# Kernel tuning notes

Measured on AMD Instinct MI355X. Metric: run time of the kernel, lower is better.

Reference implementation:

```python
import jax, jax.numpy as jnp
import numpy as np

B = 256          # batch
MID = 16384      # mid_siz
OUT = 16384      # out_siz
C = 16           # channel_siz
NLVL = 8         # nlvl (== klvl here since floor(log2(OUT/2))=13 >= 8)
MIDF = MID >> NLVL   # mid_filter_siz = 64
OUTF = OUT >> NLVL   # out_filter_siz = 64
NB = 1 << NLVL       # 256 leaf branches
STD = 0.5


def setup_inputs() -> dict:
    key = jax.random.key(0)
    ks = jax.random.split(key, 6)
    in_data = jax.random.normal(ks[0], (B, MID, 2), jnp.float32)
    # learned parameters (buildRand: normal(0, 0.5) filters, zero biases)
    mid_dense = jax.random.normal(ks[1], (1, MID, 2), jnp.float32) * STD
    in_filter = jax.random.normal(ks[2], (MIDF, 1, C), jnp.float32) * STD   # conv1d [width,in,out]
    in_bias = jnp.zeros((C,), jnp.float32)
    # level lvl (1..NLVL) uses filters[lvl-1, :2**lvl]; padded to NB branches
    filters = jax.random.normal(ks[3], (NLVL, NB, 2, C, C), jnp.float32) * STD
    biases = jnp.zeros((NLVL, NB, C), jnp.float32)
    fea_dense = jax.random.normal(ks[4], (NB, C, OUTF), jnp.float32) * STD
    return dict(in_data=in_data, mid_dense=mid_dense, in_filter=in_filter,
                in_bias=in_bias, filters=filters, biases=biases, fea_dense=fea_dense)


def reference(in_data, mid_dense, in_filter, in_bias, filters, biases, fea_dense):
    # elementwise modulation then split real/imag channels: (B, 2, MID)
    x = jnp.moveaxis(in_data * mid_dense, -1, 1)
    # level-0 conv1d: kernel MIDF, stride MIDF//2 -> overlapping half-windows.
    # Split signal into half-width chunks h; window t = [h[t], h[t+1]].
    half = MIDF // 2
    h = x.reshape(B, 2, MID // half, half)                 # (B,2,512,32)
    W1 = in_filter[:half, 0, :]                            # (32,C)
    W2 = in_filter[half:, 0, :]
    s = jnp.einsum('bisw,wc->bisc', h[:, :, :-1], W1) \
        + jnp.einsum('bisw,wc->bisc', h[:, :, 1:], W2)
    s = jax.nn.relu(s + in_bias)                           # (B,2,2^(n+1)-1,C)
    state = s[:, :, None]                                  # (B,2,nb=1,L,C)
    # butterfly tree: each level doubles branches; conv kernel=2, stride=2, VALID
    for lvl in range(1, NLVL + 1):
        nb = 1 << lvl
        p = jnp.repeat(state, 2, axis=2)                   # child itk <- parent itk//2
        L = p.shape[3]                                     # odd: 2^(n+1-lvl+1)-1
        xw = p[:, :, :, :L - 1, :].reshape(B, 2, nb, (L - 1) // 2, 2, C)
        W = filters[lvl - 1, :nb]                          # (nb,2,C,C)
        bb = biases[lvl - 1, :nb]                          # (nb,C)
        state = jax.nn.relu(
            jnp.einsum('bintkc,nkcd->bintd', xw, W) + bb[None, None, :, None, :])
    feat = state[:, :, :, 0, :]                            # (B,2,NB,C): L==1 at last level
    outp = jnp.einsum('binc,ncf->binf', feat, fea_dense)   # per-branch dense projection
    R = outp[:, 0].reshape(B, OUT // 2, 2)
    I = outp[:, 1].reshape(B, OUT // 2, 2)
    out_data = ((R[:, :, 0] - I[:, :, 1]) / MID).reshape(B, OUT // 2, 1)
    return out_data, R[:, :, 1]
```

## Files before the change

### kernel.cpp

```cpp
#include <hip/hip_runtime.h>


#define OUT_HALF 2097152

typedef __attribute__((ext_vector_type(4))) float f32x4;
typedef __attribute__((ext_vector_type(8))) short s16x8;

__device__ __forceinline__ uint fsw(uint a) {
    return a ^ ((((a >> 6) ^ (a >> 8)) & 3u) << 4);
}
__device__ __forceinline__ ushort bfr(float f) {
    uint u = __float_as_uint(f);
    return (ushort)((u + 0x7FFFu + ((u >> 16) & 1u)) >> 16);
}
__device__ __forceinline__ uint pk(float a, float b) {
    return (uint)bfr(a) | ((uint)bfr(b) << 16);
}

__device__ __forceinline__ void tree_level(
    char* smb, const int lane, const int wave,
    uint AOff, uint NOff, int lgR, int lgNP, int nTiles,
    uint WOff, int wnb, uint LBOff, int bnb)
{
    const int m  = lane & 15;
    const int kg = lane >> 4;
    const int lgTPP = lgR - 4;
    for (int at = wave; at < nTiles; at += 4) {
        const int p  = at >> lgTPP;
        const int tc = at & ((1 << lgTPP) - 1);
        const int np = p & ((1 << lgNP) - 1);
        const int ii = p >> lgNP;
        s16x8 af = *(const s16x8*)(smb + AOff + (p << (lgR + 6)) +
                                   fsw((uint)((tc * 16 + m) * 64 + kg * 16)));
#pragma unroll
        for (int sib = 0; sib < 2; sib++) {
            const int nl = 2 * np + sib;
            s16x8 bf = *(const s16x8*)(smb + WOff +
                         fsw((uint)((wnb + nl) * 1024 + m * 64 + kg * 16)));
            float bv = *(const float*)(smb + LBOff + ((bnb + nl) * 16 + m) * 4);
            f32x4 acc = {bv, bv, bv, bv};
            acc = __builtin_amdgcn_mfma_f32_16x16x32_bf16(af, bf, acc, 0, 0, 0);
            const int p2 = (ii << (lgNP + 1)) + nl;
            const uint wb = NOff + (p2 << (lgR + 5));
            const int r2 = tc * 8 + kg * 2;
            *(uint*)(smb + wb + fsw((uint)(r2 * 64 + m * 4))) =
                pk(fmaxf(acc.x, 0.f), fmaxf(acc.y, 0.f));
            *(uint*)(smb + wb + fsw((uint)((r2 + 1) * 64 + m * 4))) =
                pk(fmaxf(acc.z, 0.f), fmaxf(acc.w, 0.f));
        }
    }
}

__global__ __launch_bounds__(256, 3)
void ibf_A(const float* __restrict__ in_data, const float* __restrict__ mid_dense,
           const float* __restrict__ in_filter, const float* __restrict__ in_bias,
           const float* __restrict__ filters, const float* __restrict__ biases,
           uint* __restrict__ S3)
{
    __shared__ __align__(16) char smb[42048];
    const int tid = threadIdx.x, lane = tid & 63, wave = tid >> 6;
    const int b = blockIdx.x, th = blockIdx.y;

    {
        const float4* inb = (const float4*)in_data + (size_t)b * 8192 + th * 2048;
        const float4* mdb = (const float4*)mid_dense + th * 2048;
        for (int mp = tid; mp < 2064; mp += 256) {
            float4 iv = inb[mp], mv = mdb[mp];
            *(uint*)(smb + 0    + fsw((uint)(mp * 4))) = pk(iv.x * mv.x, iv.z * mv.z);
            *(uint*)(smb + 8256 + fsw((uint)(mp * 4))) = pk(iv.y * mv.y, iv.w * mv.w);
        }
    }
    for (int t = tid; t < 3584; t += 256) {
        int nidx = t >> 8, r = t & 255, d = r & 15, c = r >> 4;
        int lvl = (nidx < 2) ? 1 : ((nidx < 6) ? 2 : 3);
        int n = nidx - ((1 << lvl) - 2);
        const float* src = filters + (size_t)(lvl - 1) * 131072 + n * 512 + c * 16 + d;
        *(uint*)(smb + 24704 + fsw((uint)(nidx * 1024 + d * 64 + c * 4))) = pk(src[0], src[256]);
    }
    for (int t = tid; t < 512; t += 256) {
        int c = t >> 5, w2 = t & 31;
        *(uint*)(smb + 39040 + fsw((uint)(c * 128 + w2 * 4))) =
            pk(in_filter[(2 * w2) * 16 + c], in_filter[(2 * w2 + 1) * 16 + c]);
    }
    if (tid < 240) {
        float v;
        if (tid < 224) {
            int nidx = tid >> 4;
            int lvl = (nidx < 2) ? 1 : ((nidx < 6) ? 2 : 3);
            int n = nidx - ((1 << lvl) - 2);
            v = biases[(size_t)(lvl - 1) * 4096 + n * 16 + (tid & 15)];
        } else v = in_bias[tid - 224];
        *(float*)(smb + 41088 + tid * 4) = v;
    }
    __syncthreads();

    {
        const int m = lane & 15, kg = lane >> 4;
        s16x8 b0 = *(const s16x8*)(smb + 39040 + fsw((uint)(m * 128 + kg * 16)));
        s16x8 b1 = *(const s16x8*)(smb + 39040 + fsw((uint)(m * 128 + 64 + kg * 16)));
        float bv = *(const float*)(smb + 41088 + (224 + m) * 4);
        for (int at = wave; at < 16; at += 4) {
            int i = at >> 3, tc = at & 7;
            uint xb = i ? 8256u : 0u;
            s16x8 a0 = *(const s16x8*)(smb + xb + fsw((uint)((tc * 16 + m) * 64 + kg * 16)));
            s16x8 a1 = *(const s16x8*)(smb + xb + fsw((uint)((tc * 16 + m) * 64 + 64 + kg * 16)));
            f32x4 acc = {bv, bv, bv, bv};
            acc = __builtin_amdgcn_mfma_f32_16x16x32_bf16(a0, b0, acc, 0, 0, 0);
            acc = __builtin_amdgcn_mfma_f32_16x16x32_bf16(a1, b1, acc, 0, 0, 0);
            uint wb = 16512u + (uint)i * 4096u;
            int r2 = tc * 8 + kg * 2;
            *(uint*)(smb + wb + fsw((uint)(r2 * 64 + m * 4))) =
                pk(fmaxf(acc.x, 0.f), fmaxf(acc.y, 0.f));
            *(uint*)(smb + wb + fsw((uint)((r2 + 1) * 64 + m * 4))) =
                pk(fmaxf(acc.z, 0.f), fmaxf(acc.w, 0.f));
        }
    }
    __syncthreads();
    tree_level(smb, lane, wave, 16512, 0,    6, 0, 8, 24704, 0, 41088, 0);
    __syncthreads();
    tree_level(smb, lane, wave, 0,     8256, 5, 1, 8, 24704, 2, 41088, 2);
    __syncthreads();
    {
        const int m = lane & 15, kg = lane >> 4;
        for (int at = wave; at < 8; at += 4) {
            int np = at & 3, i = at >> 2;
            s16x8 af = *(const s16x8*)(smb + 8256 + (at << 10) + fsw((uint)(m * 64 + kg * 16)));
#pragma unroll
            for (int sib = 0; sib < 2; sib++) {
                int n3 = 2 * np + sib;
                s16x8 bf = *(const s16x8*)(smb + 24704 +
                             fsw((uint)((6 + n3) * 1024 + m * 64 + kg * 16)));
                float bv = *(const float*)(smb + 41088 + ((6 + n3) * 16 + m) * 4);
                f32x4 acc = {bv, bv, bv, bv};
                acc = __builtin_amdgcn_mfma_f32_16x16x32_bf16(af, bf, acc, 0, 0, 0);
                int bi = 2 * b + i;
                int t4 = th * 8 + kg * 2;
                uint idx = ((uint)(n3 * 512 + bi) * 16 + t4) * 16 + m;
                S3[idx]      = pk(fmaxf(acc.x, 0.f), fmaxf(acc.y, 0.f));
                S3[idx + 16] = pk(fmaxf(acc.z, 0.f), fmaxf(acc.w, 0.f));
            }
        }
    }
}

__global__ __launch_bounds__(256, 2)
void ibf_B(const float* __restrict__ filters, const float* __restrict__ biases,
           const float* __restrict__ fea_dense, const uint* __restrict__ S3,
           float* __restrict__ out)
{
    __shared__ __align__(16) char smb[69504];
    const int tid = threadIdx.x, lane = tid & 63, wave = tid >> 6;
    const int n3 = blockIdx.x, chunk = blockIdx.y;

    for (int o = tid * 16; o < 16384; o += 4096)
        *(float4*)(smb + 16384 + o) = make_float4(0.f, 0.f, 0.f, 0.f);
    {
        const char* src = (const char*)S3 + ((size_t)n3 * 512 + chunk * 8) * 1024;
        for (int ci = tid; ci < 512; ci += 256)
            *(float4*)(smb + fsw((uint)(ci * 16))) = *(const float4*)(src + ci * 16);
    }
    for (int t = tid; t < 992; t += 256) {
        int nidx = t >> 4, q = nidx + 2;
        int l3 = 31 - __clz(q);
        int nl = q - (1 << l3);
        int gn = (n3 << l3) + nl;
        *(float*)(smb + 65536 + t * 4) = biases[(size_t)(l3 + 2) * 4096 + gn * 16 + (t & 15)];
    }
    auto stage_w = [&](int l3) {
        int NL = 1 << l3;
        const float* fb = filters + (size_t)(l3 + 2) * 131072;
        for (int t = tid; t < NL * 256; t += 256) {
            int nl = t >> 8, r = t & 255, d = r & 15, c = r >> 4;
            const float* src = fb + (size_t)((n3 << l3) + nl) * 512 + c * 16 + d;
            *(uint*)(smb + 32768 + fsw((uint)(nl * 1024 + d * 64 + c * 4))) = pk(src[0], src[256]);
        }
    };
    stage_w(1);
    __syncthreads();
    tree_level(smb, lane, wave, 0,    8192, 7, 0, 8, 32768, 0, 65536, 0);
    __syncthreads();
    stage_w(2);
    __syncthreads();
    tree_level(smb, lane, wave, 8192, 0,    6, 1, 8, 32768, 0, 65536, 2);
    __syncthreads();
    stage_w(3);
    __syncthreads();
    tree_level(smb, lane, wave, 0,    8192, 5, 2, 8, 32768, 0, 65536, 6);
    __syncthreads();
    stage_w(4);
    __syncthreads();
    tree_level(smb, lane, wave, 8192, 0,    4, 3, 8, 32768, 0, 65536, 14);
    __syncthreads();
    stage_w(5);
    __syncthreads();
    {
        const int m = lane & 15, kg = lane >> 4;
        for (int at = wave; at < 16; at += 4) {
            s16x8 af = *(const s16x8*)(smb + at * 512 + fsw((uint)(m * 64 + kg * 16)));
#pragma unroll
            for (int sib = 0; sib < 2; sib++) {
                int nl = 2 * at + sib;
                s16x8 bf = *(const s16x8*)(smb + 32768 +
                             fsw((uint)(nl * 1024 + m * 64 + kg * 16)));
                float bv = *(const float*)(smb + 65536 + ((30 + nl) * 16 + m) * 4);
                f32x4 acc = {bv, bv, bv, bv};
                acc = __builtin_amdgcn_mfma_f32_16x16x32_bf16(af, bf, acc, 0, 0, 0);
                if (kg < 2) {
                    float v[4] = {fmaxf(acc.x, 0.f), fmaxf(acc.y, 0.f),
                                  fmaxf(acc.z, 0.f), fmaxf(acc.w, 0.f)};
#pragma unroll
                    for (int j = 0; j < 4; j++) {
                        uint o = (uint)(nl * 512 + (kg * 4 + j) * 64 + m * 2);
                        *(ushort*)(smb + 16384 + fsw(o)) = bfr(v[j]);
                    }
                }
            }
        }
    }
    __syncthreads();
    {
        const int m = lane & 15, kg = lane >> 4;
        for (int q = 0; q < 8; q++) {
            int n8l = wave * 8 + q;
            int gn8 = n3 * 32 + n8l;
            s16x8 af = *(const s16x8*)(smb + 16384 +
                         fsw((uint)(n8l * 512 + m * 64 + kg * 16)));
            const float* fb = fea_dense + (size_t)gn8 * 1024;
#pragma unroll
            for (int ut = 0; ut < 4; ut++) {
                s16x8 bf = {0, 0, 0, 0, 0, 0, 0, 0};
                if (kg < 2) {
                    const float* fp = fb + kg * 512 + ut * 16 + m;
                    bf[0] = (short)bfr(fp[0]);   bf[1] = (short)bfr(fp[64]);
                    bf[2] = (short)bfr(fp[128]); bf[3] = (short)bfr(fp[192]);
                    bf[4] = (short)bfr(fp[256]); bf[5] = (short)bfr(fp[320]);
                    bf[6] = (short)bfr(fp[384]); bf[7] = (short)bfr(fp[448]);
                }
                f32x4 acc = {0.f, 0.f, 0.f, 0.f};
                acc = __builtin_amdgcn_mfma_f32_16x16x32_bf16(af, bf, acc, 0, 0, 0);
                float s0 = __shfl_xor(acc.y, 1);
                float s2 = __shfl_xor(acc.w, 1);
                if (kg < 2) {
                    int g = gn8 * 32 + ut * 8 + (m >> 1);
                    bool odd = (m & 1);
                    float v0 = odd ? acc.x : (acc.x - s0) * (1.f / 16384.f);
                    float v1 = odd ? acc.z : (acc.z - s2) * (1.f / 16384.f);
                    size_t off = (odd ? (size_t)OUT_HALF : (size_t)0) + (size_t)g;
                    int b0 = chunk * 4 + kg * 2;
                    out[(size_t)b0 * 8192 + off]       = v0;
                    out[(size_t)(b0 + 1) * 8192 + off] = v1;
                }
            }
        }
    }
}

extern "C" void kernel_launch(void* const* d_in, const int* in_sizes, int n_in,
                              void* d_out, int out_size, void* d_ws, size_t ws_size,
                              hipStream_t stream) {
    const float* in_data   = (const float*)d_in[0];
    const float* mid_dense = (const float*)d_in[1];
    const float* in_filter = (const float*)d_in[2];
    const float* in_bias   = (const float*)d_in[3];
    const float* filters   = (const float*)d_in[4];
    const float* biases    = (const float*)d_in[5];
    const float* fea_dense = (const float*)d_in[6];
    float* out = (float*)d_out;
    uint* S3   = (uint*)d_ws;

    ibf_A<<<dim3(256, 2), 256, 0, stream>>>(in_data, mid_dense, in_filter, in_bias,
                                            filters, biases, S3);
    ibf_B<<<dim3(8, 64), 256, 0, stream>>>(filters, biases, fea_dense, S3, out);
}
```

Measured before the change: 40.31 us.

## Split final dense projection into separate kernel with LDS-staged fea_dense

Moves the per-branch dense projection out of ibf_B into a new kernel ibf_C. ibf_B now writes the leaf features to a workspace buffer, which also lets it drop the zero-fill and use less shared memory. ibf_C stages each branch's fea_dense slice into LDS once as bf16 and keeps the B fragments in registers across batch tiles. This replaces the strided global fea_dense reads that ibf_B repeated per chunk, at the cost of an extra kernel launch and a global round trip for the features. The bf16 conversion now uses the HIP intrinsic instead of hand-written rounding.

```diff
diff --git a/kernel.cpp b/kernel.cpp
--- a/kernel.cpp
+++ b/kernel.cpp
@@ -1,4 +1,5 @@
 #include <hip/hip_runtime.h>
+#include <hip/hip_bf16.h>
 
 
 #define OUT_HALF 2097152
@@ -10,8 +11,8 @@
     return a ^ ((((a >> 6) ^ (a >> 8)) & 3u) << 4);
 }
 __device__ __forceinline__ ushort bfr(float f) {
-    uint u = __float_as_uint(f);
-    return (ushort)((u + 0x7FFFu + ((u >> 16) & 1u)) >> 16);
+    __hip_bfloat16 h = __float2bfloat16(f);
+    union { __hip_bfloat16 h; ushort u; } cv; cv.h = h; return cv.u;
 }
 __device__ __forceinline__ uint pk(float a, float b) {
     return (uint)bfr(a) | ((uint)bfr(b) << 16);
@@ -121,7 +122,7 @@
     tree_level(smb, lane, wave, 0,     8256, 5, 1, 8, 24704, 2, 41088, 2);
     __syncthreads();
     {
-        const int m = lane & 15, kg = lane >> 4;
+        const int m = lane & 63 & 15, kg = (lane & 63) >> 4;
         for (int at = wave; at < 8; at += 4) {
             int np = at & 3, i = at >> 2;
             s16x8 af = *(const s16x8*)(smb + 8256 + (at << 10) + fsw((uint)(m * 64 + kg * 16)));
@@ -145,15 +146,12 @@
 
 __global__ __launch_bounds__(256, 2)
 void ibf_B(const float* __restrict__ filters, const float* __restrict__ biases,
-           const float* __restrict__ fea_dense, const uint* __restrict__ S3,
-           float* __restrict__ out)
-{
-    __shared__ __align__(16) char smb[69504];
+           const uint* __restrict__ S3, char* __restrict__ S8)
+{
+    __shared__ __align__(16) char smb[61312];
     const int tid = threadIdx.x, lane = tid & 63, wave = tid >> 6;
     const int n3 = blockIdx.x, chunk = blockIdx.y;
 
-    for (int o = tid * 16; o < 16384; o += 4096)
-        *(float4*)(smb + 16384 + o) = make_float4(0.f, 0.f, 0.f, 0.f);
     {
         const char* src = (const char*)S3 + ((size_t)n3 * 512 + chunk * 8) * 1024;
         for (int ci = tid; ci < 512; ci += 256)
@@ -164,7 +162,7 @@
         int l3 = 31 - __clz(q);
         int nl = q - (1 << l3);
         int gn = (n3 << l3) + nl;
-        *(float*)(smb + 65536 + t * 4) = biases[(size_t)(l3 + 2) * 4096 + gn * 16 + (t & 15)];
+        *(float*)(smb + 57344 + t * 4) = biases[(size_t)(l3 + 2) * 4096 + gn * 16 + (t & 15)];
     }
     auto stage_w = [&](int l3) {
         int NL = 1 << l3;
@@ -172,24 +170,24 @@
         for (int t = tid; t < NL * 256; t += 256) {
             int nl = t >> 8, r = t & 255, d = r & 15, c = r >> 4;
             const float* src = fb + (size_t)((n3 << l3) + nl) * 512 + c * 16 + d;
-            *(uint*)(smb + 32768 + fsw((uint)(nl * 1024 + d * 64 + c * 4))) = pk(src[0], src[256]);
+            *(uint*)(smb + 24576 + fsw((uint)(nl * 1024 + d * 64 + c * 4))) = pk(src[0], src[256]);
         }
     };
     stage_w(1);
     __syncthreads();
-    tree_level(smb, lane, wave, 0,    8192, 7, 0, 8, 32768, 0, 65536, 0);
+    tree_level(smb, lane, wave, 0,    8192, 7, 0, 8, 24576, 0, 57344, 0);
     __syncthreads();
     stage_w(2);
     __syncthreads();
-    tree_level(smb, lane, wave, 8192, 0,    6, 1, 8, 32768, 0, 65536, 2);
+    tree_level(smb, lane, wave, 8192, 0,    6, 1, 8, 24576, 0, 57344, 2);
     __syncthreads();
     stage_w(3);
     __syncthreads();
-    tree_level(smb, lane, wave, 0,    8192, 5, 2, 8, 32768, 0, 65536, 6);
+    tree_level(smb, lane, wave, 0,    8192, 5, 2, 8, 24576, 0, 57344, 6);
     __syncthreads();
     stage_w(4);
     __syncthreads();
-    tree_level(smb, lane, wave, 8192, 0,    4, 3, 8, 32768, 0, 65536, 14);
+    tree_level(smb, lane, wave, 8192, 0,    4, 3, 8, 24576, 0, 57344, 14);
     __syncthreads();
     stage_w(5);
     __syncthreads();
@@ -200,57 +198,72 @@
 #pragma unroll
             for (int sib = 0; sib < 2; sib++) {
                 int nl = 2 * at + sib;
-                s16x8 bf = *(const s16x8*)(smb + 32768 +
+                s16x8 bf = *(const s16x8*)(smb + 24576 +
                              fsw((uint)(nl * 1024 + m * 64 + kg * 16)));
-                float bv = *(const float*)(smb + 65536 + ((30 + nl) * 16 + m) * 4);
+                float bv = *(const float*)(smb + 57344 + ((30 + nl) * 16 + m) * 4);
                 f32x4 acc = {bv, bv, bv, bv};
                 acc = __builtin_amdgcn_mfma_f32_16x16x32_bf16(af, bf, acc, 0, 0, 0);
                 if (kg < 2) {
                     float v[4] = {fmaxf(acc.x, 0.f), fmaxf(acc.y, 0.f),
                                   fmaxf(acc.z, 0.f), fmaxf(acc.w, 0.f)};
 #pragma unroll
-                    for (int j = 0; j < 4; j++) {
-                        uint o = (uint)(nl * 512 + (kg * 4 + j) * 64 + m * 2);
-                        *(ushort*)(smb + 16384 + fsw(o)) = bfr(v[j]);
-                    }
+                    for (int j = 0; j < 4; j++)
+                        *(ushort*)(smb + 16384 + nl * 256 + (kg * 4 + j) * 32 + m * 2) = bfr(v[j]);
                 }
             }
         }
     }
     __syncthreads();
     {
-        const int m = lane & 15, kg = lane >> 4;
-        for (int q = 0; q < 8; q++) {
-            int n8l = wave * 8 + q;
-            int gn8 = n3 * 32 + n8l;
-            s16x8 af = *(const s16x8*)(smb + 16384 +
-                         fsw((uint)(n8l * 512 + m * 64 + kg * 16)));
-            const float* fb = fea_dense + (size_t)gn8 * 1024;
-#pragma unroll
-            for (int ut = 0; ut < 4; ut++) {
-                s16x8 bf = {0, 0, 0, 0, 0, 0, 0, 0};
-                if (kg < 2) {
-                    const float* fp = fb + kg * 512 + ut * 16 + m;
-                    bf[0] = (short)bfr(fp[0]);   bf[1] = (short)bfr(fp[64]);
-                    bf[2] = (short)bfr(fp[128]); bf[3] = (short)bfr(fp[192]);
-                    bf[4] = (short)bfr(fp[256]); bf[5] = (short)bfr(fp[320]);
-                    bf[6] = (short)bfr(fp[384]); bf[7] = (short)bfr(fp[448]);
-                }
-                f32x4 acc = {0.f, 0.f, 0.f, 0.f};
-                acc = __builtin_amdgcn_mfma_f32_16x16x32_bf16(af, bf, acc, 0, 0, 0);
-                float s0 = __shfl_xor(acc.y, 1);
-                float s2 = __shfl_xor(acc.w, 1);
-                if (kg < 2) {
-                    int g = gn8 * 32 + ut * 8 + (m >> 1);
-                    bool odd = (m & 1);
-                    float v0 = odd ? acc.x : (acc.x - s0) * (1.f / 16384.f);
-                    float v1 = odd ? acc.z : (acc.z - s2) * (1.f / 16384.f);
-                    size_t off = (odd ? (size_t)OUT_HALF : (size_t)0) + (size_t)g;
-                    int b0 = chunk * 4 + kg * 2;
-                    out[(size_t)b0 * 8192 + off]       = v0;
-                    out[(size_t)(b0 + 1) * 8192 + off] = v1;
-                }
-            }
+        float4* dst = (float4*)(S8 + (size_t)(n3 * 64 + chunk) * 8192);
+        for (int ci = tid; ci < 512; ci += 256)
+            dst[ci] = *(const float4*)(smb + 16384 + ci * 16);
+    }
+}
+
+__global__ __launch_bounds__(128, 8)
+void ibf_C(const float* __restrict__ fea_dense, const char* __restrict__ S8,
+           float* __restrict__ out)
+{
+    __shared__ ushort FEb[1024];
+    const int tid = threadIdx.x, lane = tid & 63, wave = tid >> 6;
+    const int n8g = blockIdx.x, half = blockIdx.y;
+    const int n3 = n8g >> 5, n8l = n8g & 31;
+
+    for (int idx = tid; idx < 1024; idx += 128) {
+        int c = idx >> 6, u = idx & 63;
+        FEb[u * 16 + c] = bfr(fea_dense[(size_t)n8g * 1024 + idx]);
+    }
+    __syncthreads();
+
+    const int m = lane & 15, kg = lane >> 4;
+    s16x8 bfrg[4];
+#pragma unroll
+    for (int ut = 0; ut < 4; ut++) {
+        if (kg < 2) bfrg[ut] = *(const s16x8*)(FEb + (ut * 16 + m) * 16 + kg * 8);
+        else        bfrg[ut] = (s16x8){0, 0, 0, 0, 0, 0, 0, 0};
+    }
+    for (int w8 = 0; w8 < 8; w8++) {
+        const int tile  = half * 16 + wave * 8 + w8;
+        const int birow = tile * 16 + m;
+        s16x8 af = {0, 0, 0, 0, 0, 0, 0, 0};
+        if (kg < 2)
+            af = *(const s16x8*)(S8 + ((size_t)(n3 * 64 + (birow >> 3)) * 32 + n8l) * 256
+                                 + (birow & 7) * 32 + kg * 16);
+        const int b0  = (tile * 16 + kg * 4) >> 1;
+        const bool odd = (m & 1);
+#pragma unroll
+        for (int ut = 0; ut < 4; ut++) {
+            f32x4 acc = {0.f, 0.f, 0.f, 0.f};
+            acc = __builtin_amdgcn_mfma_f32_16x16x32_bf16(af, bfrg[ut], acc, 0, 0, 0);
+            float sy = __shfl_xor(acc.y, 1);
+            float sw = __shfl_xor(acc.w, 1);
+            const int g = n8g * 32 + ut * 8 + (m >> 1);
+            float v0 = odd ? acc.x : (acc.x - sy) * (1.f / 16384.f);
+            float v1 = odd ? acc.z : (acc.z - sw) * (1.f / 16384.f);
+            size_t off = (odd ? (size_t)OUT_HALF : (size_t)0) + (size_t)g;
+            out[(size_t)b0 * 8192 + off]       = v0;
+            out[(size_t)(b0 + 1) * 8192 + off] = v1;
         }
     }
 }
@@ -267,8 +280,10 @@
     const float* fea_dense = (const float*)d_in[6];
     float* out = (float*)d_out;
     uint* S3   = (uint*)d_ws;
+    char* S8   = (char*)d_ws + (4 << 20);
 
     ibf_A<<<dim3(256, 2), 256, 0, stream>>>(in_data, mid_dense, in_filter, in_bias,
                                             filters, biases, S3);
-    ibf_B<<<dim3(8, 64), 256, 0, stream>>>(filters, biases, fea_dense, S3, out);
-}
+    ibf_B<<<dim3(8, 64), 256, 0, stream>>>(filters, biases, S3, S8);
+    ibf_C<<<dim3(256, 2), 128, 0, stream>>>(fea_dense, S8, out);
+}
```

After: 40.63 us. About the same (+0.8%).
